# Performance work log

Hardware: AMD Instinct MI355X
Metric: run time of the kernel (lower is better)

Reference implementation:

```python
import jax, jax.numpy as jnp
import numpy as np

N_NODES = 100000
N_EDGES = 600000
N_GRAPHS = 4096
F_IN = 74
H = 128
L = 3
BN_EPS = 1e-5


def setup_inputs() -> dict:
    key = jax.random.key(0)
    ks = jax.random.split(key, 12)
    x = jax.random.normal(ks[0], (N_NODES, F_IN), dtype=jnp.float32)
    edge_index = jax.random.randint(ks[1], (2, N_EDGES), 0, N_NODES)
    batch = jnp.sort(jax.random.randint(ks[2], (N_NODES,), 0, N_GRAPHS))

    def lin(k, fan_in, fan_out):
        return (jax.random.normal(k, (fan_in, fan_out), dtype=jnp.float32)
                / np.float32(np.sqrt(fan_in)))

    emb_W = lin(ks[3], F_IN, H)
    emb_b = jnp.zeros((H,), jnp.float32)
    conv_W = jax.random.normal(ks[4], (L, H, H), dtype=jnp.float32) / np.float32(np.sqrt(H))
    conv_b = jnp.zeros((L, H), jnp.float32)
    bn_gamma = jnp.ones((L, H), jnp.float32)
    bn_beta = jnp.zeros((L, H), jnp.float32)
    w1 = lin(ks[5], 2 * H, H)
    b1 = jnp.zeros((H,), jnp.float32)
    w2 = lin(ks[6], H, H // 2)
    b2 = jnp.zeros((H // 2,), jnp.float32)
    w3 = lin(ks[7], H // 2, 1)
    b3 = jnp.zeros((1,), jnp.float32)
    return dict(x=x, edge_index=edge_index, batch=batch,
                emb_W=emb_W, emb_b=emb_b, conv_W=conv_W, conv_b=conv_b,
                bn_gamma=bn_gamma, bn_beta=bn_beta,
                w1=w1, b1=b1, w2=w2, b2=b2, w3=w3, b3=b3)


def reference(x, edge_index, batch, emb_W, emb_b, conv_W, conv_b,
              bn_gamma, bn_beta, w1, b1, w2, b2, w3, b3):
    N = x.shape[0]
    # GCN normalization with self-loops (PyG GCNConv semantics)
    loops = jnp.arange(N)
    src = jnp.concatenate([edge_index[0], loops])  # [E+N]
    dst = jnp.concatenate([edge_index[1], loops])
    deg = jax.ops.segment_sum(jnp.ones_like(dst, jnp.float32), dst, num_segments=N)
    dinv = jax.lax.rsqrt(jnp.maximum(deg, 1.0))  # deg >= 1 due to self-loops
    norm = dinv[src] * dinv[dst]                 # [E+N]

    h = jax.nn.relu(x @ emb_W + emb_b)           # [N, H]
    for i in range(L):
        hw = h @ conv_W[i]                       # [N, H]
        msg = hw[src] * norm[:, None]            # gather + scale  [E+N, H]
        h = jax.ops.segment_sum(msg, dst, num_segments=N) + conv_b[i]
        # BatchNorm1d, training-mode batch statistics (biased variance)
        mu = jnp.mean(h, axis=0)
        var = jnp.mean((h - mu) ** 2, axis=0)
        h = (h - mu) * jax.lax.rsqrt(var + BN_EPS) * bn_gamma[i] + bn_beta[i]
        h = jax.nn.relu(h)
        # dropout: identity (inference / deterministic baseline)

    # segment mean / max pooling over graphs
    cnt = jax.ops.segment_sum(jnp.ones((N,), jnp.float32), batch, num_segments=N_GRAPHS)
    g_mean = jax.ops.segment_sum(h, batch, num_segments=N_GRAPHS) / jnp.maximum(cnt, 1.0)[:, None]
    g_max = jax.ops.segment_max(h, batch, num_segments=N_GRAPHS)
    g_max = jnp.where(jnp.isfinite(g_max), g_max, 0.0)  # guard empty segments
    g = jnp.concatenate([g_mean, g_max], axis=1)         # [G, 2H]

    h1 = jax.nn.relu(g @ w1 + b1)
    h2 = jax.nn.relu(h1 @ w2 + b2)
    return h2 @ w3 + b3                                   # [G, 1]
```

## Files before the change

kernel.cpp:

```cpp
#include <hip/hip_runtime.h>

#define NN 100000
#define NE 600000
#define NG 4096
#define FIN 74
#define HD 128
#define NL 3
#define BN_EPS 1e-5f
#define NSCAN 391
#define NHISTB 2344

typedef __attribute__((ext_vector_type(8))) short short8;
typedef __attribute__((ext_vector_type(4))) float floatx4;
typedef __attribute__((ext_vector_type(8))) unsigned short bf16x8;
typedef __attribute__((ext_vector_type(4))) unsigned short bf16x4;

__device__ __forceinline__ unsigned short f2bf(float f) {
    unsigned u = __float_as_uint(f);
    u += 0x7fff + ((u >> 16) & 1);
    return (unsigned short)(u >> 16);
}
__device__ __forceinline__ float bf2f(unsigned short u) {
    return __uint_as_float(((unsigned)u) << 16);
}

__global__ __launch_bounds__(256) void k_pre(const int* __restrict__ dst,
                                             int* __restrict__ degi,
                                             const int* __restrict__ batch,
                                             int* __restrict__ gstart,
                                             const float* __restrict__ embW,
                                             const float* __restrict__ convW,
                                             unsigned short* __restrict__ WfE,
                                             unsigned short* __restrict__ WfC) {
    int blk = blockIdx.x;
    int t = threadIdx.x;
    if (blk < NHISTB) {
        int e = blk * 256 + t;
        if (e < NE) atomicAdd(&degi[dst[e]], 1);
    } else if (blk < NHISTB + NSCAN) {
        int n = (blk - NHISTB) * 256 + t;
        if (n >= NN) return;
        int b = batch[n];
        int bp = (n == 0) ? -1 : batch[n - 1];
        for (int g = bp + 1; g <= b; g++) gstart[g] = n;
        if (n == NN - 1)
            for (int g = b + 1; g <= NG; g++) gstart[g] = NN;
    } else {
        int d = (blk - NHISTB - NSCAN) * 256 + t;
        if (d < 12288) {
            int inner = d & 511, outer = d >> 9;
            int kstep = outer % 3, nt = outer / 3;
            int g = inner >> 7, n = (inner >> 3) & 15, j = inner & 7;
            int k = kstep * 32 + g * 8 + j;
            float v = (k < FIN) ? embW[k * HD + nt * 16 + n] : 0.0f;
            WfE[d] = f2bf(v);
        } else {
            int e = d - 12288;
            if (e >= NL * 16384) return;
            int layer = e >> 14, r = e & 16383;
            int j = r & 7, n = (r >> 3) & 15, g = (r >> 7) & 3, kstep = (r >> 9) & 3, nt = r >> 11;
            int k = kstep * 32 + g * 8 + j;
            WfC[e] = f2bf(convW[layer * 16384 + k * HD + nt * 16 + n]);
        }
    }
}

__global__ __launch_bounds__(256) void k_scan1(const int* __restrict__ degi,
                                               int* __restrict__ part) {
    __shared__ int s[256];
    int t = threadIdx.x;
    int idx = blockIdx.x * 256 + t;
    s[t] = (idx < NN) ? degi[idx] : 0;
    __syncthreads();
    for (int off = 128; off > 0; off >>= 1) {
        if (t < off) s[t] += s[t + off];
        __syncthreads();
    }
    if (t == 0) part[blockIdx.x] = s[0];
}

__global__ __launch_bounds__(512) void k_scan2(int* __restrict__ part) {
    __shared__ int s[512];
    int t = threadIdx.x;
    s[t] = (t < NSCAN) ? part[t] : 0;
    __syncthreads();
    for (int off = 1; off < 512; off <<= 1) {
        int v = s[t];
        int a = (t >= off) ? s[t - off] : 0;
        __syncthreads();
        s[t] = v + a;
        __syncthreads();
    }
    if (t < NSCAN) part[t] = (t > 0) ? s[t - 1] : 0;
}

__global__ __launch_bounds__(256) void k_scan3(const int* __restrict__ degi,
                                               const int* __restrict__ part,
                                               int* __restrict__ rowptr,
                                               float* __restrict__ dinv) {
    __shared__ int s[256];
    int t = threadIdx.x;
    int idx = blockIdx.x * 256 + t;
    int v = (idx < NN) ? degi[idx] : 0;
    s[t] = v;
    __syncthreads();
    for (int off = 1; off < 256; off <<= 1) {
        int x = s[t];
        int a = (t >= off) ? s[t - off] : 0;
        __syncthreads();
        s[t] = x + a;
        __syncthreads();
    }
    if (idx < NN) {
        rowptr[idx] = part[blockIdx.x] + (s[t] - v);
        dinv[idx] = rsqrtf((float)v + 1.0f);
    }
    if (idx == 0) rowptr[NN] = NE;
}

__global__ __launch_bounds__(256) void k_fill(const int* __restrict__ src,
                                              const int* __restrict__ dst,
                                              const int* __restrict__ rowptr,
                                              int* __restrict__ cursor,
                                              int* __restrict__ col) {
    int e = blockIdx.x * 256 + threadIdx.x;
    if (e >= NE) return;
    int d = dst[e];
    int pos = rowptr[d] + atomicAdd(&cursor[d], 1);
    col[pos] = src[e];
}

__global__ __launch_bounds__(256) void k_emb(const float* __restrict__ x,
                                             const unsigned short* __restrict__ Wf,
                                             const float* __restrict__ b,
                                             unsigned short* __restrict__ hA) {
    __shared__ __align__(16) unsigned short As[4224];
    int t = threadIdx.x;
    int n0 = blockIdx.x * 32;
    for (int f = t; f < 3072; f += 256) {
        int m = f / 96, kp = f % 96;
        float v = (kp < FIN) ? x[(n0 + m) * FIN + kp] : 0.0f;
        int kstep = kp >> 5, g = (kp >> 3) & 3, j = kp & 7;
        As[(kstep * 4 + g) * 264 + m * 8 + j] = f2bf(v);
    }
    __syncthreads();
    int lane = t & 63, wv = t >> 6;
    int lanelo = lane & 15, g = lane >> 4;
    floatx4 acc[2][2] = {};
#pragma unroll
    for (int kstep = 0; kstep < 3; kstep++) {
        short8 a0 = *(const short8*)&As[(kstep * 4 + g) * 264 + lanelo * 8];
        short8 a1 = *(const short8*)&As[(kstep * 4 + g) * 264 + 128 + lanelo * 8];
        short8 b0 = *(const short8*)&Wf[(((wv * 2 + 0) * 3 + kstep) * 4 + g) * 128 + lanelo * 8];
        short8 b1 = *(const short8*)&Wf[(((wv * 2 + 1) * 3 + kstep) * 4 + g) * 128 + lanelo * 8];
        acc[0][0] = __builtin_amdgcn_mfma_f32_16x16x32_bf16(a0, b0, acc[0][0], 0, 0, 0);
        acc[0][1] = __builtin_amdgcn_mfma_f32_16x16x32_bf16(a0, b1, acc[0][1], 0, 0, 0);
        acc[1][0] = __builtin_amdgcn_mfma_f32_16x16x32_bf16(a1, b0, acc[1][0], 0, 0, 0);
        acc[1][1] = __builtin_amdgcn_mfma_f32_16x16x32_bf16(a1, b1, acc[1][1], 0, 0, 0);
    }
    __syncthreads();
#pragma unroll
    for (int ns = 0; ns < 2; ns++) {
        int colc = wv * 32 + ns * 16 + lanelo;
        float bias = b[colc];
#pragma unroll
        for (int ms = 0; ms < 2; ms++)
#pragma unroll
            for (int r = 0; r < 4; r++) {
                int rowl = ms * 16 + g * 4 + r;
                As[rowl * 132 + colc] = f2bf(fmaxf(acc[ms][ns][r] + bias, 0.0f));
            }
    }
    __syncthreads();
#pragma unroll
    for (int i = 0; i < 2; i++) {
        int f = t * 8 + i * 2048;
        int m = f >> 7, c = f & 127;
        bf16x4 lo = *(const bf16x4*)&As[m * 132 + c];
        bf16x4 hi = *(const bf16x4*)&As[m * 132 + c + 4];
        bf16x8 o = {lo.x, lo.y, lo.z, lo.w, hi.x, hi.y, hi.z, hi.w};
        *(bf16x8*)&hA[n0 * HD + f] = o;
    }
}

template <bool BN>
__global__ __launch_bounds__(256) void k_conv(const unsigned short* __restrict__ hin,
                                              const float* __restrict__ bnsum,
                                              const float* __restrict__ gamma,
                                              const float* __restrict__ beta,
                                              const unsigned short* __restrict__ Wf,
                                              const float* __restrict__ dinv,
                                              unsigned short* __restrict__ hw) {
    __shared__ __align__(16) unsigned short As[4224];
    __shared__ float dinvs[32];
    int t = threadIdx.x;
    int n0 = blockIdx.x * 32;
    if (t < 32) dinvs[t] = dinv[n0 + t];
    int f0 = t * 8;
    int k0 = f0 & 127;
    float sc[8], sh[8];
    if (BN) {
        const float inv_n = 1.0f / (float)NN;
#pragma unroll
        for (int jj = 0; jj < 8; jj++) {
            int k = k0 + jj;
            float mu = bnsum[k] * inv_n;
            float var = bnsum[HD + k] * inv_n - mu * mu;
            float s = gamma[k] * rsqrtf(var + BN_EPS);
            sc[jj] = s;
            sh[jj] = beta[k] - mu * s;
        }
    }
    int combo = (k0 >> 5) * 4 + ((k0 >> 3) & 3);
#pragma unroll
    for (int i = 0; i < 2; i++) {
        int f = f0 + i * 2048;
        int m = f >> 7;
        bf16x8 u = *(const bf16x8*)&hin[n0 * HD + f];
        bf16x8 o;
        if (BN) {
#pragma unroll
            for (int jj = 0; jj < 8; jj++) {
                float v = fmaxf(bf2f(u[jj]) * sc[jj] + sh[jj], 0.0f);
                o[jj] = f2bf(v);
            }
        } else {
            o = u;
        }
        *(bf16x8*)&As[combo * 264 + m * 8] = o;
    }
    __syncthreads();
    int lane = t & 63, wv = t >> 6;
    int lanelo = lane & 15, g = lane >> 4;
    floatx4 acc[2][2] = {};
#pragma unroll
    for (int ks = 0; ks < 4; ks++) {
        short8 a0 = *(const short8*)&As[(ks * 4 + g) * 264 + lanelo * 8];
        short8 a1 = *(const short8*)&As[(ks * 4 + g) * 264 + 128 + lanelo * 8];
        short8 b0 = *(const short8*)&Wf[(((wv * 2 + 0) * 4 + ks) * 4 + g) * 128 + lanelo * 8];
        short8 b1 = *(const short8*)&Wf[(((wv * 2 + 1) * 4 + ks) * 4 + g) * 128 + lanelo * 8];
        acc[0][0] = __builtin_amdgcn_mfma_f32_16x16x32_bf16(a0, b0, acc[0][0], 0, 0, 0);
        acc[0][1] = __builtin_amdgcn_mfma_f32_16x16x32_bf16(a0, b1, acc[0][1], 0, 0, 0);
        acc[1][0] = __builtin_amdgcn_mfma_f32_16x16x32_bf16(a1, b0, acc[1][0], 0, 0, 0);
        acc[1][1] = __builtin_amdgcn_mfma_f32_16x16x32_bf16(a1, b1, acc[1][1], 0, 0, 0);
    }
    __syncthreads();
#pragma unroll
    for (int ms = 0; ms < 2; ms++)
#pragma unroll
        for (int ns = 0; ns < 2; ns++) {
            int colc = wv * 32 + ns * 16 + lanelo;
#pragma unroll
            for (int r = 0; r < 4; r++) {
                int rowl = ms * 16 + g * 4 + r;
                As[rowl * 132 + colc] = f2bf(acc[ms][ns][r] * dinvs[rowl]);
            }
        }
    __syncthreads();
#pragma unroll
    for (int i = 0; i < 2; i++) {
        int f = f0 + i * 2048;
        int m = f >> 7, c = f & 127;
        bf16x4 lo = *(const bf16x4*)&As[m * 132 + c];
        bf16x4 hi = *(const bf16x4*)&As[m * 132 + c + 4];
        bf16x8 o = {lo.x, lo.y, lo.z, lo.w, hi.x, hi.y, hi.z, hi.w};
        *(bf16x8*)&hw[n0 * HD + f] = o;
    }
}

__global__ __launch_bounds__(256) void k_gather(const int* __restrict__ rowptr,
                                                const int* __restrict__ col,
                                                const float* __restrict__ dinv,
                                                const unsigned short* __restrict__ B,
                                                const float* __restrict__ bias,
                                                unsigned short* __restrict__ A) {
    int t = threadIdx.x;
    int n = blockIdx.x * 16 + (t >> 4);
    int c8 = (t & 15) * 8;
    bf16x8 u = *(const bf16x8*)&B[n * HD + c8];
    float acc[8];
#pragma unroll
    for (int i = 0; i < 8; i++) acc[i] = bf2f(u[i]);
    int j0 = rowptr[n], j1 = rowptr[n + 1];
    int j = j0;
    for (; j + 1 < j1; j += 2) {
        int s0 = col[j], s1 = col[j + 1];
        bf16x8 v0 = *(const bf16x8*)&B[s0 * HD + c8];
        bf16x8 v1 = *(const bf16x8*)&B[s1 * HD + c8];
#pragma unroll
        for (int i = 0; i < 8; i++) acc[i] += bf2f(v0[i]) + bf2f(v1[i]);
    }
    if (j < j1) {
        int s = col[j];
        bf16x8 v = *(const bf16x8*)&B[s * HD + c8];
#pragma unroll
        for (int i = 0; i < 8; i++) acc[i] += bf2f(v[i]);
    }
    float dd = dinv[n];
    floatx4 b0 = *(const floatx4*)&bias[c8];
    floatx4 b1 = *(const floatx4*)&bias[c8 + 4];
    bf16x8 o;
    o[0] = f2bf(acc[0] * dd + b0.x); o[1] = f2bf(acc[1] * dd + b0.y);
    o[2] = f2bf(acc[2] * dd + b0.z); o[3] = f2bf(acc[3] * dd + b0.w);
    o[4] = f2bf(acc[4] * dd + b1.x); o[5] = f2bf(acc[5] * dd + b1.y);
    o[6] = f2bf(acc[6] * dd + b1.z); o[7] = f2bf(acc[7] * dd + b1.w);
    *(bf16x8*)&A[n * HD + c8] = o;
}

__global__ __launch_bounds__(256) void k_bn_stats(const unsigned short* __restrict__ h,
                                                  float* __restrict__ sums) {
    __shared__ float ls[256];
    int t = threadIdx.x;
    ls[t] = 0.0f;
    __syncthreads();
    int c8 = (t & 15) * 8;
    float s[8] = {}, sq[8] = {};
    for (int n = blockIdx.x * 16 + (t >> 4); n < NN; n += gridDim.x * 16) {
        bf16x8 u = *(const bf16x8*)&h[n * HD + c8];
#pragma unroll
        for (int i = 0; i < 8; i++) {
            float v = bf2f(u[i]);
            s[i] += v;
            sq[i] += v * v;
        }
    }
#pragma unroll
    for (int i = 0; i < 8; i++) {
        atomicAdd(&ls[c8 + i], s[i]);
        atomicAdd(&ls[HD + c8 + i], sq[i]);
    }
    __syncthreads();
    atomicAdd(&sums[t], ls[t]);
}

__global__ __launch_bounds__(128) void k_pool_g(const unsigned short* __restrict__ h,
                                                const float* __restrict__ bnsum,
                                                const float* __restrict__ gamma,
                                                const float* __restrict__ beta,
                                                const int* __restrict__ gstart,
                                                float* __restrict__ gfeat) {
    int g = blockIdx.x;
    int c = threadIdx.x;
    int n0 = gstart[g], n1 = gstart[g + 1];
    const float inv_n = 1.0f / (float)NN;
    float mu = bnsum[c] * inv_n;
    float var = bnsum[HD + c] * inv_n - mu * mu;
    float sc = gamma[c] * rsqrtf(var + BN_EPS);
    float sh = beta[c] - mu * sc;
    float s = 0.0f, mx = 0.0f;
    for (int n = n0; n < n1; n++) {
        float v = fmaxf(bf2f(h[n * HD + c]) * sc + sh, 0.0f);
        s += v;
        mx = fmaxf(mx, v);
    }
    float cntf = (float)(n1 - n0);
    gfeat[g * 256 + c] = s / fmaxf(cntf, 1.0f);
    gfeat[g * 256 + HD + c] = mx;
}

__global__ __launch_bounds__(256) void k_mlp(const float* __restrict__ gfeat,
                                             const float* __restrict__ w1,
                                             const float* __restrict__ b1,
                                             const float* __restrict__ w2,
                                             const float* __restrict__ b2,
                                             const float* __restrict__ w3,
                                             const float* __restrict__ b3,
                                             float* __restrict__ out) {
    __shared__ float gs[8][258];
    __shared__ float p1[8][130];
    __shared__ float hs[8][130];
    __shared__ float p2[3][8][66];
    __shared__ float h2s[8][66];
    __shared__ float ps[64];
    int t = threadIdx.x;
    int g0 = blockIdx.x * 8;
    for (int f = t; f < 2048; f += 256) {
        int gi = f >> 8, k = f & 255;
        gs[gi][k] = gfeat[(g0 + gi) * 256 + k];
    }
    __syncthreads();
    {
        int colc = t & 127, half = t >> 7;
        int kb = half * 128;
        float acc[8] = {};
        for (int k = 0; k < 128; k++) {
            float w = w1[(kb + k) * HD + colc];
#pragma unroll
            for (int gi = 0; gi < 8; gi++) acc[gi] += gs[gi][kb + k] * w;
        }
        if (half == 1) {
#pragma unroll
            for (int gi = 0; gi < 8; gi++) p1[gi][colc] = acc[gi];
        }
        __syncthreads();
        if (half == 0) {
            float bias = b1[colc];
#pragma unroll
            for (int gi = 0; gi < 8; gi++)
                hs[gi][colc] = fmaxf(acc[gi] + p1[gi][colc] + bias, 0.0f);
        }
    }
    __syncthreads();
    {
        int colc = t & 63, q = t >> 6;
        int kb = q * 32;
        float acc[8] = {};
        for (int k = 0; k < 32; k++) {
            float w = w2[(kb + k) * 64 + colc];
#pragma unroll
            for (int gi = 0; gi < 8; gi++) acc[gi] += hs[gi][kb + k] * w;
        }
        if (q > 0) {
#pragma unroll
            for (int gi = 0; gi < 8; gi++) p2[q - 1][gi][colc] = acc[gi];
        }
        __syncthreads();
        if (q == 0) {
            float bias = b2[colc];
#pragma unroll
            for (int gi = 0; gi < 8; gi++)
                h2s[gi][colc] = fmaxf(acc[gi] + p2[0][gi][colc] + p2[1][gi][colc]
                                      + p2[2][gi][colc] + bias, 0.0f);
        }
    }
    __syncthreads();
    if (t < 64) {
        int gi = t >> 3, prt = t & 7;
        float p = 0.0f;
#pragma unroll
        for (int k = 0; k < 8; k++) p += h2s[gi][prt * 8 + k] * w3[prt * 8 + k];
        ps[t] = p;
    }
    __syncthreads();
    if (t < 8) {
        float a = b3[0];
#pragma unroll
        for (int i = 0; i < 8; i++) a += ps[t * 8 + i];
        out[g0 + t] = a;
    }
}

extern "C" void kernel_launch(void* const* d_in, const int* in_sizes, int n_in,
                              void* d_out, int out_size, void* d_ws, size_t ws_size,
                              hipStream_t stream) {
    const float* x      = (const float*)d_in[0];
    const int*   eidx   = (const int*)d_in[1];
    const int*   batch  = (const int*)d_in[2];
    const float* emb_W  = (const float*)d_in[3];
    const float* emb_b  = (const float*)d_in[4];
    const float* conv_W = (const float*)d_in[5];
    const float* conv_b = (const float*)d_in[6];
    const float* gamma  = (const float*)d_in[7];
    const float* beta   = (const float*)d_in[8];
    const float* w1     = (const float*)d_in[9];
    const float* b1     = (const float*)d_in[10];
    const float* w2     = (const float*)d_in[11];
    const float* b2     = (const float*)d_in[12];
    const float* w3     = (const float*)d_in[13];
    const float* b3     = (const float*)d_in[14];
    float* out = (float*)d_out;

    const int* src = eidx;
    const int* dst = eidx + NE;

    unsigned short* A = (unsigned short*)d_ws;
    unsigned short* B = A + NN * HD;
    float* dinv  = (float*)(B + NN * HD);
    float* gfeat = dinv + NN;
    float* bnsum3= gfeat + NG * 256;
    int*   degi  = (int*)(bnsum3 + NL * 256);
    int*   cursor= degi + NN;
    int*   gstart= cursor + NN;
    int*   rowptr= gstart + NG + 1;
    int*   part  = rowptr + NN + 1;
    int*   col   = part + NSCAN;
    unsigned short* WfE = (unsigned short*)(col + NE);
    unsigned short* WfC = WfE + 12288;

    (void)hipMemsetAsync(bnsum3, 0,
                         (NL * 256) * sizeof(float) + 2 * NN * sizeof(int), stream);
    k_pre<<<NHISTB + NSCAN + 240, 256, 0, stream>>>(dst, degi, batch, gstart,
                                                    emb_W, conv_W, WfE, WfC);
    k_scan1<<<NSCAN, 256, 0, stream>>>(degi, part);
    k_scan2<<<1, 512, 0, stream>>>(part);
    k_scan3<<<NSCAN, 256, 0, stream>>>(degi, part, rowptr, dinv);
    k_fill<<<(NE + 255) / 256, 256, 0, stream>>>(src, dst, rowptr, cursor, col);

    k_emb<<<NN / 32, 256, 0, stream>>>(x, WfE, emb_b, A);

    for (int l = 0; l < NL; l++) {
        if (l == 0)
            k_conv<false><<<NN / 32, 256, 0, stream>>>(A, nullptr, nullptr, nullptr,
                                                       WfC, dinv, B);
        else
            k_conv<true><<<NN / 32, 256, 0, stream>>>(A, bnsum3 + (l - 1) * 256,
                                                      gamma + (l - 1) * HD,
                                                      beta + (l - 1) * HD,
                                                      WfC + l * 16384, dinv, B);
        k_gather<<<NN / 16, 256, 0, stream>>>(rowptr, col, dinv, B, conv_b + l * HD, A);
        k_bn_stats<<<512, 256, 0, stream>>>(A, bnsum3 + l * 256);
    }

    k_pool_g<<<NG, 128, 0, stream>>>(A, bnsum3 + 2 * 256, gamma + 2 * HD, beta + 2 * HD,
                                     gstart, gfeat);

    k_mlp<<<NG / 8, 256, 0, stream>>>(gfeat, w1, b1, w2, b2, w3, b3, out);
}
```

Measured before the change: 407.9 us.

## Fuse GCN aggregate-then-transform with BN stats into one persistent kernel per layer

Each layer now runs as one persistent kernel. It applies the previous layer's BN and ReLU on the fly while gathering neighbor rows, does the GEMM on the aggregated tile, and accumulates BN statistics in the epilogue. Using (A·H)·W instead of A·(H·W) removes the separate conv, gather and stats passes and their intermediate round trips to global memory. The BN+ReLU and dinv scaling are now recomputed for every gathered neighbor, and the atomic stat reduction is spread over eight shadow copies to cut contention.

```diff
diff --git a/kernel.cpp b/kernel.cpp
--- a/kernel.cpp
+++ b/kernel.cpp
@@ -9,6 +9,9 @@
 #define BN_EPS 1e-5f
 #define NSCAN 391
 #define NHISTB 2344
+#define NTILES 3125
+#define NSHADOW 8
+#define GRID_FUSED 1024
 
 typedef __attribute__((ext_vector_type(8))) short short8;
 typedef __attribute__((ext_vector_type(4))) float floatx4;
@@ -184,153 +187,150 @@
 }
 
 template <bool BN>
-__global__ __launch_bounds__(256) void k_conv(const unsigned short* __restrict__ hin,
-                                              const float* __restrict__ bnsum,
-                                              const float* __restrict__ gamma,
-                                              const float* __restrict__ beta,
-                                              const unsigned short* __restrict__ Wf,
-                                              const float* __restrict__ dinv,
-                                              unsigned short* __restrict__ hw) {
+__global__ __launch_bounds__(256) void k_fused(const unsigned short* __restrict__ Ain,
+                                               const int* __restrict__ rowptr,
+                                               const int* __restrict__ col,
+                                               const float* __restrict__ dinv,
+                                               const float* __restrict__ bnprev,
+                                               const float* __restrict__ gamma,
+                                               const float* __restrict__ beta,
+                                               const unsigned short* __restrict__ Wf,
+                                               const float* __restrict__ bias,
+                                               float* __restrict__ bnout,
+                                               unsigned short* __restrict__ Aout) {
     __shared__ __align__(16) unsigned short As[4224];
-    __shared__ float dinvs[32];
-    int t = threadIdx.x;
-    int n0 = blockIdx.x * 32;
-    if (t < 32) dinvs[t] = dinv[n0 + t];
-    int f0 = t * 8;
-    int k0 = f0 & 127;
+    int t = threadIdx.x;
+    int sub = t >> 4;
+    int lanec = t & 15;
+    int k0 = lanec * 8;
+
     float sc[8], sh[8];
     if (BN) {
         const float inv_n = 1.0f / (float)NN;
 #pragma unroll
         for (int jj = 0; jj < 8; jj++) {
-            int k = k0 + jj;
-            float mu = bnsum[k] * inv_n;
-            float var = bnsum[HD + k] * inv_n - mu * mu;
-            float s = gamma[k] * rsqrtf(var + BN_EPS);
-            sc[jj] = s;
-            sh[jj] = beta[k] - mu * s;
-        }
-    }
-    int combo = (k0 >> 5) * 4 + ((k0 >> 3) & 3);
-#pragma unroll
-    for (int i = 0; i < 2; i++) {
-        int f = f0 + i * 2048;
-        int m = f >> 7;
-        bf16x8 u = *(const bf16x8*)&hin[n0 * HD + f];
-        bf16x8 o;
-        if (BN) {
-#pragma unroll
-            for (int jj = 0; jj < 8; jj++) {
-                float v = fmaxf(bf2f(u[jj]) * sc[jj] + sh[jj], 0.0f);
-                o[jj] = f2bf(v);
+            int c = k0 + jj;
+            float s = 0.0f, q = 0.0f;
+#pragma unroll
+            for (int kk = 0; kk < NSHADOW; kk++) {
+                s += bnprev[kk * 256 + c];
+                q += bnprev[kk * 256 + 128 + c];
             }
-        } else {
-            o = u;
-        }
-        *(bf16x8*)&As[combo * 264 + m * 8] = o;
-    }
-    __syncthreads();
+            float mu = s * inv_n;
+            float var = q * inv_n - mu * mu;
+            float g = gamma[c] * rsqrtf(var + BN_EPS);
+            sc[jj] = g;
+            sh[jj] = beta[c] - mu * g;
+        }
+    }
+
     int lane = t & 63, wv = t >> 6;
     int lanelo = lane & 15, g = lane >> 4;
-    floatx4 acc[2][2] = {};
-#pragma unroll
-    for (int ks = 0; ks < 4; ks++) {
-        short8 a0 = *(const short8*)&As[(ks * 4 + g) * 264 + lanelo * 8];
-        short8 a1 = *(const short8*)&As[(ks * 4 + g) * 264 + 128 + lanelo * 8];
-        short8 b0 = *(const short8*)&Wf[(((wv * 2 + 0) * 4 + ks) * 4 + g) * 128 + lanelo * 8];
-        short8 b1 = *(const short8*)&Wf[(((wv * 2 + 1) * 4 + ks) * 4 + g) * 128 + lanelo * 8];
-        acc[0][0] = __builtin_amdgcn_mfma_f32_16x16x32_bf16(a0, b0, acc[0][0], 0, 0, 0);
-        acc[0][1] = __builtin_amdgcn_mfma_f32_16x16x32_bf16(a0, b1, acc[0][1], 0, 0, 0);
-        acc[1][0] = __builtin_amdgcn_mfma_f32_16x16x32_bf16(a1, b0, acc[1][0], 0, 0, 0);
-        acc[1][1] = __builtin_amdgcn_mfma_f32_16x16x32_bf16(a1, b1, acc[1][1], 0, 0, 0);
-    }
-    __syncthreads();
-#pragma unroll
-    for (int ms = 0; ms < 2; ms++)
-#pragma unroll
-        for (int ns = 0; ns < 2; ns++) {
-            int colc = wv * 32 + ns * 16 + lanelo;
-#pragma unroll
-            for (int r = 0; r < 4; r++) {
-                int rowl = ms * 16 + g * 4 + r;
-                As[rowl * 132 + colc] = f2bf(acc[ms][ns][r] * dinvs[rowl]);
+    float bias0 = bias[wv * 32 + lanelo];
+    float bias1 = bias[wv * 32 + 16 + lanelo];
+    float ssum[2] = {}, ssq[2] = {};
+
+    for (int tile = blockIdx.x; tile < NTILES; tile += gridDim.x) {
+        int n0 = tile * 32;
+#pragma unroll
+        for (int p = 0; p < 2; p++) {
+            int n = n0 + p * 16 + sub;
+            float dn = dinv[n];
+            float acc[8];
+            bf16x8 u = *(const bf16x8*)&Ain[n * HD + k0];
+#pragma unroll
+            for (int i = 0; i < 8; i++) {
+                float v = bf2f(u[i]);
+                if (BN) v = fmaxf(v * sc[i] + sh[i], 0.0f);
+                acc[i] = dn * v;
             }
-        }
-    __syncthreads();
-#pragma unroll
-    for (int i = 0; i < 2; i++) {
-        int f = f0 + i * 2048;
-        int m = f >> 7, c = f & 127;
-        bf16x4 lo = *(const bf16x4*)&As[m * 132 + c];
-        bf16x4 hi = *(const bf16x4*)&As[m * 132 + c + 4];
-        bf16x8 o = {lo.x, lo.y, lo.z, lo.w, hi.x, hi.y, hi.z, hi.w};
-        *(bf16x8*)&hw[n0 * HD + f] = o;
-    }
-}
-
-__global__ __launch_bounds__(256) void k_gather(const int* __restrict__ rowptr,
-                                                const int* __restrict__ col,
-                                                const float* __restrict__ dinv,
-                                                const unsigned short* __restrict__ B,
-                                                const float* __restrict__ bias,
-                                                unsigned short* __restrict__ A) {
-    int t = threadIdx.x;
-    int n = blockIdx.x * 16 + (t >> 4);
-    int c8 = (t & 15) * 8;
-    bf16x8 u = *(const bf16x8*)&B[n * HD + c8];
-    float acc[8];
-#pragma unroll
-    for (int i = 0; i < 8; i++) acc[i] = bf2f(u[i]);
-    int j0 = rowptr[n], j1 = rowptr[n + 1];
-    int j = j0;
-    for (; j + 1 < j1; j += 2) {
-        int s0 = col[j], s1 = col[j + 1];
-        bf16x8 v0 = *(const bf16x8*)&B[s0 * HD + c8];
-        bf16x8 v1 = *(const bf16x8*)&B[s1 * HD + c8];
-#pragma unroll
-        for (int i = 0; i < 8; i++) acc[i] += bf2f(v0[i]) + bf2f(v1[i]);
-    }
-    if (j < j1) {
-        int s = col[j];
-        bf16x8 v = *(const bf16x8*)&B[s * HD + c8];
-#pragma unroll
-        for (int i = 0; i < 8; i++) acc[i] += bf2f(v[i]);
-    }
-    float dd = dinv[n];
-    floatx4 b0 = *(const floatx4*)&bias[c8];
-    floatx4 b1 = *(const floatx4*)&bias[c8 + 4];
-    bf16x8 o;
-    o[0] = f2bf(acc[0] * dd + b0.x); o[1] = f2bf(acc[1] * dd + b0.y);
-    o[2] = f2bf(acc[2] * dd + b0.z); o[3] = f2bf(acc[3] * dd + b0.w);
-    o[4] = f2bf(acc[4] * dd + b1.x); o[5] = f2bf(acc[5] * dd + b1.y);
-    o[6] = f2bf(acc[6] * dd + b1.z); o[7] = f2bf(acc[7] * dd + b1.w);
-    *(bf16x8*)&A[n * HD + c8] = o;
-}
-
-__global__ __launch_bounds__(256) void k_bn_stats(const unsigned short* __restrict__ h,
-                                                  float* __restrict__ sums) {
-    __shared__ float ls[256];
-    int t = threadIdx.x;
+            int j = rowptr[n], j1 = rowptr[n + 1];
+            for (; j + 1 < j1; j += 2) {
+                int s0 = col[j], s1 = col[j + 1];
+                float d0 = dinv[s0], d1 = dinv[s1];
+                bf16x8 v0 = *(const bf16x8*)&Ain[s0 * HD + k0];
+                bf16x8 v1 = *(const bf16x8*)&Ain[s1 * HD + k0];
+#pragma unroll
+                for (int i = 0; i < 8; i++) {
+                    float a = bf2f(v0[i]);
+                    float b2 = bf2f(v1[i]);
+                    if (BN) {
+                        a = fmaxf(a * sc[i] + sh[i], 0.0f);
+                        b2 = fmaxf(b2 * sc[i] + sh[i], 0.0f);
+                    }
+                    acc[i] = fmaf(d0, a, acc[i]);
+                    acc[i] = fmaf(d1, b2, acc[i]);
+                }
+            }
+            if (j < j1) {
+                int s0 = col[j];
+                float d0 = dinv[s0];
+                bf16x8 v0 = *(const bf16x8*)&Ain[s0 * HD + k0];
+#pragma unroll
+                for (int i = 0; i < 8; i++) {
+                    float a = bf2f(v0[i]);
+                    if (BN) a = fmaxf(a * sc[i] + sh[i], 0.0f);
+                    acc[i] = fmaf(d0, a, acc[i]);
+                }
+            }
+            bf16x8 o;
+#pragma unroll
+            for (int i = 0; i < 8; i++) o[i] = f2bf(acc[i] * dn);
+            *(bf16x8*)&As[lanec * 264 + (p * 16 + sub) * 8] = o;
+        }
+        __syncthreads();
+        floatx4 macc[2][2] = {};
+#pragma unroll
+        for (int ks = 0; ks < 4; ks++) {
+            short8 a0 = *(const short8*)&As[(ks * 4 + g) * 264 + lanelo * 8];
+            short8 a1 = *(const short8*)&As[(ks * 4 + g) * 264 + 128 + lanelo * 8];
+            short8 b0 = *(const short8*)&Wf[(((wv * 2 + 0) * 4 + ks) * 4 + g) * 128 + lanelo * 8];
+            short8 b1 = *(const short8*)&Wf[(((wv * 2 + 1) * 4 + ks) * 4 + g) * 128 + lanelo * 8];
+            macc[0][0] = __builtin_amdgcn_mfma_f32_16x16x32_bf16(a0, b0, macc[0][0], 0, 0, 0);
+            macc[0][1] = __builtin_amdgcn_mfma_f32_16x16x32_bf16(a0, b1, macc[0][1], 0, 0, 0);
+            macc[1][0] = __builtin_amdgcn_mfma_f32_16x16x32_bf16(a1, b0, macc[1][0], 0, 0, 0);
+            macc[1][1] = __builtin_amdgcn_mfma_f32_16x16x32_bf16(a1, b1, macc[1][1], 0, 0, 0);
+        }
+        __syncthreads();
+#pragma unroll
+        for (int ms = 0; ms < 2; ms++)
+#pragma unroll
+            for (int ns = 0; ns < 2; ns++) {
+                int colc = wv * 32 + ns * 16 + lanelo;
+                float bb = ns ? bias1 : bias0;
+#pragma unroll
+                for (int r = 0; r < 4; r++) {
+                    int rowl = ms * 16 + g * 4 + r;
+                    float v = macc[ms][ns][r] + bb;
+                    ssum[ns] += v;
+                    ssq[ns] += v * v;
+                    As[rowl * 132 + colc] = f2bf(v);
+                }
+            }
+        __syncthreads();
+#pragma unroll
+        for (int i = 0; i < 2; i++) {
+            int f = t * 8 + i * 2048;
+            int m = f >> 7, c = f & 127;
+            bf16x4 lo = *(const bf16x4*)&As[m * 132 + c];
+            bf16x4 hi = *(const bf16x4*)&As[m * 132 + c + 4];
+            bf16x8 o = {lo.x, lo.y, lo.z, lo.w, hi.x, hi.y, hi.z, hi.w};
+            *(bf16x8*)&Aout[n0 * HD + f] = o;
+        }
+        __syncthreads();
+    }
+    float* ls = (float*)As;
     ls[t] = 0.0f;
     __syncthreads();
-    int c8 = (t & 15) * 8;
-    float s[8] = {}, sq[8] = {};
-    for (int n = blockIdx.x * 16 + (t >> 4); n < NN; n += gridDim.x * 16) {
-        bf16x8 u = *(const bf16x8*)&h[n * HD + c8];
-#pragma unroll
-        for (int i = 0; i < 8; i++) {
-            float v = bf2f(u[i]);
-            s[i] += v;
-            sq[i] += v * v;
-        }
-    }
-#pragma unroll
-    for (int i = 0; i < 8; i++) {
-        atomicAdd(&ls[c8 + i], s[i]);
-        atomicAdd(&ls[HD + c8 + i], sq[i]);
-    }
-    __syncthreads();
-    atomicAdd(&sums[t], ls[t]);
+    {
+        int colc0 = wv * 32 + lanelo;
+        atomicAdd(&ls[colc0], ssum[0]);
+        atomicAdd(&ls[128 + colc0], ssq[0]);
+        atomicAdd(&ls[colc0 + 16], ssum[1]);
+        atomicAdd(&ls[128 + colc0 + 16], ssq[1]);
+    }
+    __syncthreads();
+    atomicAdd(&bnout[(blockIdx.x & (NSHADOW - 1)) * 256 + t], ls[t]);
 }
 
 __global__ __launch_bounds__(128) void k_pool_g(const unsigned short* __restrict__ h,
@@ -343,8 +343,14 @@
     int c = threadIdx.x;
     int n0 = gstart[g], n1 = gstart[g + 1];
     const float inv_n = 1.0f / (float)NN;
-    float mu = bnsum[c] * inv_n;
-    float var = bnsum[HD + c] * inv_n - mu * mu;
+    float s0 = 0.0f, q0 = 0.0f;
+#pragma unroll
+    for (int k = 0; k < NSHADOW; k++) {
+        s0 += bnsum[k * 256 + c];
+        q0 += bnsum[k * 256 + 128 + c];
+    }
+    float mu = s0 * inv_n;
+    float var = q0 * inv_n - mu * mu;
     float sc = gamma[c] * rsqrtf(var + BN_EPS);
     float sh = beta[c] - mu * sc;
     float s = 0.0f, mx = 0.0f;
@@ -468,7 +474,7 @@
     float* dinv  = (float*)(B + NN * HD);
     float* gfeat = dinv + NN;
     float* bnsum3= gfeat + NG * 256;
-    int*   degi  = (int*)(bnsum3 + NL * 256);
+    int*   degi  = (int*)(bnsum3 + NL * NSHADOW * 256);
     int*   cursor= degi + NN;
     int*   gstart= cursor + NN;
     int*   rowptr= gstart + NG + 1;
@@ -478,7 +484,8 @@
     unsigned short* WfC = WfE + 12288;
 
     (void)hipMemsetAsync(bnsum3, 0,
-                         (NL * 256) * sizeof(float) + 2 * NN * sizeof(int), stream);
+                         (NL * NSHADOW * 256) * sizeof(float) + 2 * NN * sizeof(int),
+                         stream);
     k_pre<<<NHISTB + NSCAN + 240, 256, 0, stream>>>(dst, degi, batch, gstart,
                                                     emb_W, conv_W, WfE, WfC);
     k_scan1<<<NSCAN, 256, 0, stream>>>(degi, part);
@@ -488,20 +495,21 @@
 
     k_emb<<<NN / 32, 256, 0, stream>>>(x, WfE, emb_b, A);
 
-    for (int l = 0; l < NL; l++) {
-        if (l == 0)
-            k_conv<false><<<NN / 32, 256, 0, stream>>>(A, nullptr, nullptr, nullptr,
-                                                       WfC, dinv, B);
-        else
-            k_conv<true><<<NN / 32, 256, 0, stream>>>(A, bnsum3 + (l - 1) * 256,
-                                                      gamma + (l - 1) * HD,
-                                                      beta + (l - 1) * HD,
-                                                      WfC + l * 16384, dinv, B);
-        k_gather<<<NN / 16, 256, 0, stream>>>(rowptr, col, dinv, B, conv_b + l * HD, A);
-        k_bn_stats<<<512, 256, 0, stream>>>(A, bnsum3 + l * 256);
-    }
-
-    k_pool_g<<<NG, 128, 0, stream>>>(A, bnsum3 + 2 * 256, gamma + 2 * HD, beta + 2 * HD,
+    k_fused<false><<<GRID_FUSED, 256, 0, stream>>>(A, rowptr, col, dinv,
+                                                   nullptr, nullptr, nullptr,
+                                                   WfC, conv_b, bnsum3, B);
+    k_fused<true><<<GRID_FUSED, 256, 0, stream>>>(B, rowptr, col, dinv,
+                                                  bnsum3, gamma, beta,
+                                                  WfC + 16384, conv_b + HD,
+                                                  bnsum3 + NSHADOW * 256, A);
+    k_fused<true><<<GRID_FUSED, 256, 0, stream>>>(A, rowptr, col, dinv,
+                                                  bnsum3 + NSHADOW * 256,
+                                                  gamma + HD, beta + HD,
+                                                  WfC + 2 * 16384, conv_b + 2 * HD,
+                                                  bnsum3 + 2 * NSHADOW * 256, B);
+
+    k_pool_g<<<NG, 128, 0, stream>>>(B, bnsum3 + 2 * NSHADOW * 256,
+                                     gamma + 2 * HD, beta + 2 * HD,
                                      gstart, gfeat);
 
     k_mlp<<<NG / 8, 256, 0, stream>>>(gfeat, w1, b1, w2, b2, w3, b3, out);
```

Result: faster. 392.0 us (-3.9%).
